# Kernel optimization log

Measured on AMD Instinct MI355X. Metric: run time of the kernel, lower is better.

Reference implementation:

```python
import jax, jax.numpy as jnp
import numpy as np


def fps(xyz, npoint):
    # farthest point sampling, starts at index 0 (matches pointnet2 CUDA kernel)
    B, N, _ = xyz.shape
    def step(carry, _):
        min_d, last = carry
        last_xyz = jnp.take_along_axis(xyz, last[:, None, None], axis=1)  # [B,1,3]
        d = jnp.sum((xyz - last_xyz) ** 2, axis=-1)                        # [B,N]
        min_d = jnp.minimum(min_d, d)
        nxt = jnp.argmax(min_d, axis=1).astype(jnp.int32)
        return (min_d, nxt), last
    init = (jnp.full((B, N), 1e10, xyz.dtype), jnp.zeros((B,), jnp.int32))
    _, idx = jax.lax.scan(step, init, None, length=npoint)
    return jnp.transpose(idx)  # [B, npoint]


def ball_query(xyz, new_xyz, radius, nsample):
    # first nsample points within radius; pad with first hit (0 if none) -- CUDA semantics
    N = xyz.shape[1]
    d2 = jnp.sum((new_xyz[:, :, None, :] - xyz[:, None, :, :]) ** 2, axis=-1)  # [B,S,N]
    cand = jnp.where(d2 < radius * radius, jnp.arange(N, dtype=jnp.int32)[None, None, :], N)
    srt = jnp.sort(cand, axis=-1)[..., :nsample]
    first = srt[..., :1]
    first = jnp.where(first == N, 0, first)
    return jnp.where(srt == N, first, srt)  # [B,S,K]


def gather_nbrs(x, idx):
    # x [B,N,C], idx [B,S,K] -> [B,S,K,C]
    B, S, K = idx.shape
    flat = jnp.take_along_axis(x, idx.reshape(B, S * K, 1), axis=1)
    return flat.reshape(B, S, K, x.shape[-1])


def shared_mlp(x, layers):
    # 1x1 conv (+ folded eval-mode BN) + ReLU per layer
    for w, b in layers:
        x = jax.nn.relu(jnp.einsum('bskc,oc->bsko', x, w) + b)
    return x


def sa_module(xyz, feat, npoint, radius, nsample, layers):
    idx = fps(xyz, npoint)
    new_xyz = jnp.take_along_axis(xyz, idx[:, :, None], axis=1)  # [B,S,3]
    gidx = ball_query(xyz, new_xyz, radius, nsample)
    grouped = gather_nbrs(xyz, gidx) - new_xyz[:, :, None, :]    # centered local xyz
    if feat is not None:
        grouped = jnp.concatenate([grouped, gather_nbrs(feat, gidx)], axis=-1)
    x = shared_mlp(grouped, layers)
    return new_xyz, jnp.max(x, axis=2)  # max-pool over neighbors -> [B,S,Cout]


def sa_module_all(xyz, feat, layers):
    # GroupAll: concat raw (uncentered) xyz with features, one group of all points
    x = jnp.concatenate([xyz, feat], axis=-1)[:, None]  # [B,1,N,3+C]
    x = shared_mlp(x, layers)
    return jnp.max(x, axis=2)[:, 0]  # [B,Cout]


def _forward(data, ws):
    B, T, N, _ = data.shape
    xyz = data.reshape(B * T, N, 3)
    xyz, feat = sa_module(xyz, None, 256, 0.2, 32, ws[0])
    xyz, feat = sa_module(xyz, feat, 128, 0.4, 32, ws[1])
    out = sa_module_all(xyz, feat, ws[2])
    return out.reshape(B, T, -1)


DIMS = [(3, 64), (64, 64), (64, 128), (131, 128), (128, 128), (128, 256), (259, 256), (256, 512), (512, 1024)]
NAMES = ['1_0', '1_1', '1_2', '2_0', '2_1', '2_2', '3_0', '3_1', '3_2']


def setup_inputs() -> dict:
    key = jax.random.key(0)
    keys = jax.random.split(key, 1 + 2 * len(DIMS))
    inp = {'data': jax.random.normal(keys[0], (4, 8, 4096, 3), jnp.float32)}
    for i, ((cin, cout), nm) in enumerate(zip(DIMS, NAMES)):
        inp['w' + nm] = jax.random.normal(keys[1 + 2 * i], (cout, cin), jnp.float32) / np.sqrt(cin).astype(np.float32)
        inp['b' + nm] = jax.random.normal(keys[2 + 2 * i], (cout,), jnp.float32) * 0.02
    return inp


def reference(data, w1_0, b1_0, w1_1, b1_1, w1_2, b1_2,
              w2_0, b2_0, w2_1, b2_1, w2_2, b2_2,
              w3_0, b3_0, w3_1, b3_1, w3_2, b3_2):
    ws = [[(w1_0, b1_0), (w1_1, b1_1), (w1_2, b1_2)],
          [(w2_0, b2_0), (w2_1, b2_1), (w2_2, b2_2)],
          [(w3_0, b3_0), (w3_1, b3_1), (w3_2, b3_2)]]
    return _forward(data, ws)
```

## Files before the change

kernel.cpp:

```cpp
#include <hip/hip_runtime.h>
#include <hip/hip_bf16.h>
#include <cstdint>
#include <cstddef>

#define BT 32
#define N1 4096
#define S1 256
#define S2 128
#define KNB 32

typedef __attribute__((ext_vector_type(8))) short short8;
typedef __attribute__((ext_vector_type(4))) float f32x4;

__device__ __forceinline__ float sqdist(float ax, float ay, float az,
                                        float bx, float by, float bz) {
    float dx = __fsub_rn(ax, bx), dy = __fsub_rn(ay, by), dz = __fsub_rn(az, bz);
    return __fadd_rn(__fadd_rn(__fmul_rn(dx, dx), __fmul_rn(dy, dy)), __fmul_rn(dz, dz));
}

__device__ __forceinline__ unsigned short f2bf(float f) {
    unsigned u = __float_as_uint(f);
    return (unsigned short)((u + 0x7FFFu + ((u >> 16) & 1u)) >> 16);
}
__device__ __forceinline__ float bf2f(unsigned short h) {
    return __uint_as_float(((unsigned)h) << 16);
}

__device__ __forceinline__ unsigned long long packvi(float v, int idx) {
    return ((unsigned long long)__float_as_uint(v) << 32) | (unsigned)(~idx);
}

template <int CTRL>
__device__ __forceinline__ unsigned long long dppmax(unsigned long long v) {
    int lo = (int)(unsigned)(v & 0xFFFFFFFFull);
    int hi = (int)(unsigned)(v >> 32);
    int lo2 = __builtin_amdgcn_update_dpp(0, lo, CTRL, 0xF, 0xF, false);
    int hi2 = __builtin_amdgcn_update_dpp(0, hi, CTRL, 0xF, 0xF, false);
    unsigned long long o = ((unsigned long long)(unsigned)hi2 << 32) | (unsigned)lo2;
    return o > v ? o : v;
}
template <int CTRL>
__device__ __forceinline__ void redstep(unsigned long long& v, float& x, float& y, float& z) {
    int lo2 = __builtin_amdgcn_update_dpp(0, (int)(unsigned)(v & 0xFFFFFFFFull), CTRL, 0xF, 0xF, false);
    int hi2 = __builtin_amdgcn_update_dpp(0, (int)(unsigned)(v >> 32), CTRL, 0xF, 0xF, false);
    int x2 = __builtin_amdgcn_update_dpp(0, __float_as_int(x), CTRL, 0xF, 0xF, false);
    int y2 = __builtin_amdgcn_update_dpp(0, __float_as_int(y), CTRL, 0xF, 0xF, false);
    int z2 = __builtin_amdgcn_update_dpp(0, __float_as_int(z), CTRL, 0xF, 0xF, false);
    unsigned long long o = ((unsigned long long)(unsigned)hi2 << 32) | (unsigned)(unsigned)lo2;
    if (o > v) { v = o; x = __int_as_float(x2); y = __int_as_float(y2); z = __int_as_float(z2); }
}
#define ROR1 0x121
#define ROR2 0x122
#define ROR4 0x124
#define ROR8 0x128

__global__ __launch_bounds__(256) void fps1_kernel(const float* __restrict__ xyz,
                                                   float* __restrict__ nxz,
                                                   float* __restrict__ nxz2) {
    const int b = blockIdx.x, tid = threadIdx.x;
    const int lane = tid & 63, wv = tid >> 6;
    const float* X = xyz + (size_t)b * (N1 * 3);
    __shared__ float4 s4[N1];
    __shared__ unsigned long long slots_v[2][16];
    __shared__ float4 slots_c[2][16];
    __shared__ float hist[S1 * 3];
    __shared__ float4 shist[S1];
    float px[16], py[16], pz[16], md[16];
    int bidx[16];
#pragma unroll
    for (int j = 0; j < 16; ++j) {
        int i = tid + 256 * j;
        float x = X[i * 3 + 0], y = X[i * 3 + 1], z = X[i * 3 + 2];
        s4[i] = make_float4(x, y, z, 0.f);
        px[j] = x; py[j] = y; pz[j] = z;
        md[j] = 1e10f;
        bidx[j] = i;
    }
    if (tid == 0) { hist[0] = X[0]; hist[1] = X[1]; hist[2] = X[2]; }
    __syncthreads();
    float lx = X[0], ly = X[1], lz = X[2];
    for (int t = 1; t < S1; ++t) {
        float bv = -1.0f; int bi = 0;
#pragma unroll
        for (int j = 0; j < 16; ++j) {
            float d = sqdist(px[j], py[j], pz[j], lx, ly, lz);
            float m = fminf(md[j], d);
            md[j] = m;
            if (m > bv) { bv = m; bi = bidx[j]; }
        }
        unsigned long long best = packvi(bv, bi);
        best = dppmax<ROR1>(best);
        best = dppmax<ROR2>(best);
        best = dppmax<ROR4>(best);
        best = dppmax<ROR8>(best);
        if ((lane & 15) == 0) {
            int vi = (int)(~(unsigned)best);
            slots_v[t & 1][wv * 4 + (lane >> 4)] = best;
            slots_c[t & 1][wv * 4 + (lane >> 4)] = s4[vi];
        }
        __syncthreads();
        unsigned long long v = slots_v[t & 1][lane & 15];
        float4 c = slots_c[t & 1][lane & 15];
        float x = c.x, y = c.y, z = c.z;
        redstep<ROR1>(v, x, y, z);
        redstep<ROR2>(v, x, y, z);
        redstep<ROR4>(v, x, y, z);
        redstep<ROR8>(v, x, y, z);
        lx = x; ly = y; lz = z;
        if (tid == 0) { hist[t * 3 + 0] = lx; hist[t * 3 + 1] = ly; hist[t * 3 + 2] = lz; }
    }
    __syncthreads();
    for (int u = tid; u < S1 * 3; u += 256) nxz[(size_t)b * S1 * 3 + u] = hist[u];
    if (wv == 0) {
        float p2x[4], p2y[4], p2z[4], m2[4];
        int b2i[4];
#pragma unroll
        for (int j = 0; j < 4; ++j) {
            int i = lane + 64 * j;
            float x = hist[i * 3 + 0], y = hist[i * 3 + 1], z = hist[i * 3 + 2];
            shist[i] = make_float4(x, y, z, 0.f);
            p2x[j] = x; p2y[j] = y; p2z[j] = z;
            m2[j] = 1e10f;
            b2i[j] = i;
        }
        if (lane == 0) {
            nxz2[(size_t)b * S2 * 3 + 0] = hist[0];
            nxz2[(size_t)b * S2 * 3 + 1] = hist[1];
            nxz2[(size_t)b * S2 * 3 + 2] = hist[2];
        }
        float cx = hist[0], cy = hist[1], cz = hist[2];
        for (int t = 1; t < S2; ++t) {
            float bv = -1.0f; int bi = 0;
#pragma unroll
            for (int j = 0; j < 4; ++j) {
                float d = sqdist(p2x[j], p2y[j], p2z[j], cx, cy, cz);
                float m = fminf(m2[j], d);
                m2[j] = m;
                if (m > bv) { bv = m; bi = b2i[j]; }
            }
            unsigned long long best = packvi(bv, bi);
            best = dppmax<ROR1>(best);
            best = dppmax<ROR2>(best);
            best = dppmax<ROR4>(best);
            best = dppmax<ROR8>(best);
            { unsigned long long o = __shfl_xor(best, 16); best = o > best ? o : best; }
            { unsigned long long o = __shfl_xor(best, 32); best = o > best ? o : best; }
            int vi = (int)(~(unsigned)best);
            float4 c = shist[vi];
            cx = c.x; cy = c.y; cz = c.z;
            if (lane == 0) {
                float* dst = nxz2 + ((size_t)b * S2 + t) * 3;
                dst[0] = cx; dst[1] = cy; dst[2] = cz;
            }
        }
    }
}

__global__ __launch_bounds__(256) void ballq1_kernel(const float* __restrict__ xyz,
                                                     const float* __restrict__ nxz,
                                                     int* __restrict__ gidx) {
    const int wid = (blockIdx.x * 256 + threadIdx.x) >> 6;
    const int lane = threadIdx.x & 63;
    const int b = wid >> 8;
    const float* X = xyz + (size_t)b * (N1 * 3);
    const float* C = nxz + (size_t)wid * 3;
    const float cx = C[0], cy = C[1], cz = C[2];
    const float r2 = (float)(0.2 * 0.2);
    int* G = gidx + (size_t)wid * KNB;
    int cnt = 0, first = 0;
    bool found = false;
    for (int j0 = 0; j0 < N1 && cnt < KNB; j0 += 64) {
        int j = j0 + lane;
        float d2 = sqdist(cx, cy, cz, X[j * 3 + 0], X[j * 3 + 1], X[j * 3 + 2]);
        bool hit = d2 < r2;
        unsigned long long mask = __ballot(hit);
        if (!found && mask) { first = j0 + __builtin_ctzll(mask); found = true; }
        if (hit) {
            int pos = cnt + __popcll(mask & ((1ull << lane) - 1ull));
            if (pos < KNB) G[pos] = j;
        }
        cnt += __popcll(mask);
    }
    if (cnt < KNB) {
        int pad = found ? first : 0;
        if (lane >= cnt && lane < KNB) G[lane] = pad;
    }
}

__global__ __launch_bounds__(256) void ballq2_kernel(const float* __restrict__ xyz1,
                                                     const float* __restrict__ nxz2,
                                                     int* __restrict__ gidx) {
    const int wid = (blockIdx.x * 256 + threadIdx.x) >> 6;
    const int lane = threadIdx.x & 63;
    const int b = wid >> 7;
    const float* X = xyz1 + (size_t)b * (S1 * 3);
    const float* C = nxz2 + (size_t)wid * 3;
    const float cx = C[0], cy = C[1], cz = C[2];
    const float r2 = (float)(0.4 * 0.4);
    int* G = gidx + (size_t)wid * KNB;
    int cnt = 0, first = 0;
    bool found = false;
    for (int j0 = 0; j0 < S1 && cnt < KNB; j0 += 64) {
        int j = j0 + lane;
        float d2 = sqdist(cx, cy, cz, X[j * 3 + 0], X[j * 3 + 1], X[j * 3 + 2]);
        bool hit = d2 < r2;
        unsigned long long mask = __ballot(hit);
        if (!found && mask) { first = j0 + __builtin_ctzll(mask); found = true; }
        if (hit) {
            int pos = cnt + __popcll(mask & ((1ull << lane) - 1ull));
            if (pos < KNB) G[pos] = j;
        }
        cnt += __popcll(mask);
    }
    if (cnt < KNB) {
        int pad = found ? first : 0;
        if (lane >= cnt && lane < KNB) G[lane] = pad;
    }
}

__global__ __launch_bounds__(256) void wconv_kernel(
    const float* __restrict__ w11, const float* __restrict__ w12,
    const float* __restrict__ w20, const float* __restrict__ w21,
    const float* __restrict__ w22, const float* __restrict__ w30,
    const float* __restrict__ w31, const float* __restrict__ w32,
    unsigned short* __restrict__ wb) {
    int u = blockIdx.x * 256 + threadIdx.x;
    if (u >= 823296) return;
    const float* src; int base, Kp, Ko; int perm = 0;
    if      (u < 4096)   { src = w11; base = 0;      Kp = 64;  Ko = 64;  }
    else if (u < 12288)  { src = w12; base = 4096;   Kp = 64;  Ko = 64;  }
    else if (u < 36864)  { src = w20; base = 12288;  Kp = 192; Ko = 131; perm = 128; }
    else if (u < 53248)  { src = w21; base = 36864;  Kp = 128; Ko = 128; }
    else if (u < 86016)  { src = w22; base = 53248;  Kp = 128; Ko = 128; }
    else if (u < 167936) { src = w30; base = 86016;  Kp = 320; Ko = 259; perm = 256; }
    else if (u < 299008) { src = w31; base = 167936; Kp = 256; Ko = 256; }
    else                 { src = w32; base = 299008; Kp = 512; Ko = 512; }
    int local = u - base;
    int n = local / Kp, k = local - n * Kp;
    float v;
    if (perm) {
        int ksrc = (k < perm) ? (k + 3) : ((k < perm + 3) ? (k - perm) : -1);
        v = (ksrc >= 0) ? src[(size_t)n * Ko + ksrc] : 0.f;
    } else {
        v = (k < Ko) ? src[(size_t)n * Ko + k] : 0.f;
    }
    wb[u] = f2bf(v);
}

__global__ __launch_bounds__(256) void m1_kernel(
    const float* __restrict__ xyz, const float* __restrict__ nxz,
    const int* __restrict__ g1,
    const float* __restrict__ w10, const float* __restrict__ b10,
    const unsigned short* __restrict__ w11b, const float* __restrict__ b11,
    const unsigned short* __restrict__ w12b, const float* __restrict__ b12,
    unsigned short* __restrict__ f1) {
    constexpr int AP = 72;
    __shared__ __align__(16) unsigned short As[128 * AP];
    __shared__ __align__(16) unsigned short Hs[128 * AP];
    __shared__ __align__(16) unsigned short Bs[128 * AP];
    __shared__ float sxyz[128 * 3];
    const int t = threadIdx.x;
    const int lane = t & 63, w = t >> 6;
    const int r16 = lane & 15, q = lane >> 4;
    const int m0 = blockIdx.x * 128;

    if (t < 128) {
        int row = m0 + t, bs = row >> 5, b = bs >> 8, j = g1[row];
        const float* P = xyz + ((size_t)b * N1 + j) * 3;
        const float* Cc = nxz + (size_t)bs * 3;
        sxyz[t * 3 + 0] = P[0] - Cc[0];
        sxyz[t * 3 + 1] = P[1] - Cc[1];
        sxyz[t * 3 + 2] = P[2] - Cc[2];
    }
    for (int c = t; c < 64 * 8; c += 256) {
        int row = c >> 3, ch = c & 7;
        *(short8*)&Bs[row * AP + ch * 8] = *(const short8*)&w11b[row * 64 + ch * 8];
    }
    __syncthreads();
    {
        const int r = t >> 1, half = (t & 1) * 32;
        const float x = sxyz[r * 3 + 0], y = sxyz[r * 3 + 1], z = sxyz[r * 3 + 2];
        unsigned short tmp[32];
#pragma unroll
        for (int o = 0; o < 32; ++o) {
            int oo = half + o;
            float acc = b10[oo];
            acc = fmaf(x, w10[oo * 3 + 0], acc);
            acc = fmaf(y, w10[oo * 3 + 1], acc);
            acc = fmaf(z, w10[oo * 3 + 2], acc);
            tmp[o] = f2bf(fmaxf(acc, 0.f));
        }
#pragma unroll
        for (int c2 = 0; c2 < 4; ++c2)
            *(short8*)&As[r * AP + half + c2 * 8] = *(short8*)&tmp[c2 * 8];
    }
    __syncthreads();
    {
        f32x4 acc[2][4];
#pragma unroll
        for (int i = 0; i < 2; ++i)
#pragma unroll
            for (int j = 0; j < 4; ++j) acc[i][j] = (f32x4){0.f, 0.f, 0.f, 0.f};
#pragma unroll
        for (int kk = 0; kk < 64; kk += 32) {
            short8 a0 = *(const short8*)&As[(w * 32 + r16) * AP + kk + q * 8];
            short8 a1 = *(const short8*)&As[(w * 32 + 16 + r16) * AP + kk + q * 8];
#pragma unroll
            for (int j = 0; j < 4; ++j) {
                short8 bf = *(const short8*)&Bs[(j * 16 + r16) * AP + kk + q * 8];
                acc[0][j] = __builtin_amdgcn_mfma_f32_16x16x32_bf16(a0, bf, acc[0][j], 0, 0, 0);
                acc[1][j] = __builtin_amdgcn_mfma_f32_16x16x32_bf16(a1, bf, acc[1][j], 0, 0, 0);
            }
        }
#pragma unroll
        for (int i = 0; i < 2; ++i)
#pragma unroll
            for (int j = 0; j < 4; ++j) {
                int col = j * 16 + r16;
                float bv = b11[col];
#pragma unroll
                for (int r = 0; r < 4; ++r) {
                    int row = w * 32 + i * 16 + q * 4 + r;
                    Hs[row * AP + col] = f2bf(fmaxf(acc[i][j][r] + bv, 0.f));
                }
            }
    }
    __syncthreads();
    for (int c = t; c < 128 * 8; c += 256) {
        int row = c >> 3, ch = c & 7;
        *(short8*)&Bs[row * AP + ch * 8] = *(const short8*)&w12b[row * 64 + ch * 8];
    }
    __syncthreads();
    {
        f32x4 acc[2][8];
#pragma unroll
        for (int i = 0; i < 2; ++i)
#pragma unroll
            for (int j = 0; j < 8; ++j) acc[i][j] = (f32x4){0.f, 0.f, 0.f, 0.f};
#pragma unroll
        for (int kk = 0; kk < 64; kk += 32) {
            short8 a0 = *(const short8*)&Hs[(w * 32 + r16) * AP + kk + q * 8];
            short8 a1 = *(const short8*)&Hs[(w * 32 + 16 + r16) * AP + kk + q * 8];
#pragma unroll
            for (int j = 0; j < 8; ++j) {
                short8 bf = *(const short8*)&Bs[(j * 16 + r16) * AP + kk + q * 8];
                acc[0][j] = __builtin_amdgcn_mfma_f32_16x16x32_bf16(a0, bf, acc[0][j], 0, 0, 0);
                acc[1][j] = __builtin_amdgcn_mfma_f32_16x16x32_bf16(a1, bf, acc[1][j], 0, 0, 0);
            }
        }
#pragma unroll
        for (int j = 0; j < 8; ++j) {
            int col = j * 16 + r16;
            float bv = b12[col];
            float mv = 0.f;
#pragma unroll
            for (int i = 0; i < 2; ++i)
#pragma unroll
                for (int r = 0; r < 4; ++r)
                    mv = fmaxf(mv, acc[i][j][r] + bv);
            mv = fmaxf(mv, __shfl_xor(mv, 16));
            mv = fmaxf(mv, __shfl_xor(mv, 32));
            if (q == 0)
                f1[(size_t)((m0 >> 5) + w) * 128 + col] = f2bf(mv);
        }
    }
}

__global__ __launch_bounds__(256) void m2_kernel(
    const float* __restrict__ xyz1, const float* __restrict__ nxz2,
    const int* __restrict__ g2, const unsigned short* __restrict__ f1,
    const unsigned short* __restrict__ w20p, const float* __restrict__ b20,
    const unsigned short* __restrict__ w21b, const float* __restrict__ b21,
    const unsigned short* __restrict__ w22b, const float* __restrict__ b22,
    unsigned short* __restrict__ f2) {
    constexpr int AP = 72, HP = 136;
    __shared__ __align__(16) unsigned short smem[36864];
    unsigned short* R1 = smem;
    unsigned short* R2 = smem + 18432;
    unsigned short* As = R1;
    unsigned short* Bs = R1 + 9216;
    unsigned short* H1 = R2;
    unsigned short* H2 = R1;
    unsigned short* Bs2 = R2;
    __shared__ int ribase[128];
    __shared__ unsigned short sxb[128 * 3];
    const int t = threadIdx.x;
    const int lane = t & 63, w = t >> 6;
    const int r16 = lane & 15, q = lane >> 4;
    const int m0 = blockIdx.x * 128;

    if (t < 128) {
        int row = m0 + t, bs = row >> 5, b = bs >> 7, j = g2[row];
        ribase[t] = (b * 256 + j) * 128;
        const float* P = xyz1 + ((size_t)b * S1 + j) * 3;
        const float* Cc = nxz2 + (size_t)bs * 3;
        sxb[t * 3 + 0] = f2bf(P[0] - Cc[0]);
        sxb[t * 3 + 1] = f2bf(P[1] - Cc[1]);
        sxb[t * 3 + 2] = f2bf(P[2] - Cc[2]);
    }
    __syncthreads();

    f32x4 acc[2][8];
#pragma unroll
    for (int i = 0; i < 2; ++i)
#pragma unroll
        for (int j = 0; j < 8; ++j) acc[i][j] = (f32x4){0.f, 0.f, 0.f, 0.f};
    for (int kt = 0; kt < 3; ++kt) {
        const int k0 = kt * 64;
        if (kt < 2) {
            for (int c = t; c < 128 * 8; c += 256) {
                int row = c >> 3, ch = c & 7;
                *(short8*)&As[row * AP + ch * 8] =
                    *(const short8*)&f1[(size_t)ribase[row] + k0 + ch * 8];
            }
        } else {
            for (int c = t; c < 128 * 8; c += 256) {
                int row = c >> 3, ch = c & 7;
                short8 v = (short8){0, 0, 0, 0, 0, 0, 0, 0};
                if (ch == 0) {
                    v[0] = (short)sxb[row * 3 + 0];
                    v[1] = (short)sxb[row * 3 + 1];
                    v[2] = (short)sxb[row * 3 + 2];
                }
                *(short8*)&As[row * AP + ch * 8] = v;
            }
        }
        for (int c = t; c < 128 * 8; c += 256) {
            int row = c >> 3, ch = c & 7;
            *(short8*)&Bs[row * AP + ch * 8] =
                *(const short8*)&w20p[(size_t)row * 192 + k0 + ch * 8];
        }
        __syncthreads();
#pragma unroll
        for (int kk = 0; kk < 64; kk += 32) {
            short8 a0 = *(const short8*)&As[(w * 32 + r16) * AP + kk + q * 8];
            short8 a1 = *(const short8*)&As[(w * 32 + 16 + r16) * AP + kk + q * 8];
#pragma unroll
            for (int j = 0; j < 8; ++j) {
                short8 bf = *(const short8*)&Bs[(j * 16 + r16) * AP + kk + q * 8];
                acc[0][j] = __builtin_amdgcn_mfma_f32_16x16x32_bf16(a0, bf, acc[0][j], 0, 0, 0);
                acc[1][j] = __builtin_amdgcn_mfma_f32_16x16x32_bf16(a1, bf, acc[1][j], 0, 0, 0);
            }
        }
        __syncthreads();
    }
#pragma unroll
    for (int i = 0; i < 2; ++i)
#pragma unroll
        for (int j = 0; j < 8; ++j) {
            int col = j * 16 + r16;
            float bv = b20[col];
#pragma unroll
            for (int r = 0; r < 4; ++r) {
                int row = w * 32 + i * 16 + q * 4 + r;
                H1[row * HP + col] = f2bf(fmaxf(acc[i][j][r] + bv, 0.f));
            }
        }
    __syncthreads();

#pragma unroll
    for (int i = 0; i < 2; ++i)
#pragma unroll
        for (int j = 0; j < 8; ++j) acc[i][j] = (f32x4){0.f, 0.f, 0.f, 0.f};
    for (int kt = 0; kt < 2; ++kt) {
        const int k0 = kt * 64;
        for (int c = t; c < 128 * 8; c += 256) {
            int row = c >> 3, ch = c & 7;
            *(short8*)&As[row * AP + ch * 8] =
                *(const short8*)&w21b[(size_t)row * 128 + k0 + ch * 8];
        }
        __syncthreads();
#pragma unroll
        for (int kk = 0; kk < 64; kk += 32) {
            short8 a0 = *(const short8*)&H1[(w * 32 + r16) * HP + k0 + kk + q * 8];
            short8 a1 = *(const short8*)&H1[(w * 32 + 16 + r16) * HP + k0 + kk + q * 8];
#pragma unroll
            for (int j = 0; j < 8; ++j) {
                short8 bf = *(const short8*)&As[(j * 16 + r16) * AP + kk + q * 8];
                acc[0][j] = __builtin_amdgcn_mfma_f32_16x16x32_bf16(a0, bf, acc[0][j], 0, 0, 0);
                acc[1][j] = __builtin_amdgcn_mfma_f32_16x16x32_bf16(a1, bf, acc[1][j], 0, 0, 0);
            }
        }
        __syncthreads();
    }
#pragma unroll
    for (int i = 0; i < 2; ++i)
#pragma unroll
        for (int j = 0; j < 8; ++j) {
            int col = j * 16 + r16;
            float bv = b21[col];
#pragma unroll
            for (int r = 0; r < 4; ++r) {
                int row = w * 32 + i * 16 + q * 4 + r;
                H2[row * HP + col] = f2bf(fmaxf(acc[i][j][r] + bv, 0.f));
            }
        }
    __syncthreads();

    f32x4 acc2[2][16];
#pragma unroll
    for (int i = 0; i < 2; ++i)
#pragma unroll
        for (int j = 0; j < 16; ++j) acc2[i][j] = (f32x4){0.f, 0.f, 0.f, 0.f};
    for (int kt = 0; kt < 2; ++kt) {
        const int k0 = kt * 64;
        for (int c = t; c < 256 * 8; c += 256) {
            int row = c >> 3, ch = c & 7;
            *(short8*)&Bs2[row * AP + ch * 8] =
                *(const short8*)&w22b[(size_t)row * 128 + k0 + ch * 8];
        }
        __syncthreads();
#pragma unroll
        for (int kk = 0; kk < 64; kk += 32) {
            short8 a0 = *(const short8*)&H2[(w * 32 + r16) * HP + k0 + kk + q * 8];
            short8 a1 = *(const short8*)&H2[(w * 32 + 16 + r16) * HP + k0 + kk + q * 8];
#pragma unroll
            for (int j = 0; j < 16; ++j) {
                short8 bf = *(const short8*)&Bs2[(j * 16 + r16) * AP + kk + q * 8];
                acc2[0][j] = __builtin_amdgcn_mfma_f32_16x16x32_bf16(a0, bf, acc2[0][j], 0, 0, 0);
                acc2[1][j] = __builtin_amdgcn_mfma_f32_16x16x32_bf16(a1, bf, acc2[1][j], 0, 0, 0);
            }
        }
        __syncthreads();
    }
#pragma unroll
    for (int j = 0; j < 16; ++j) {
        int col = j * 16 + r16;
        float bv = b22[col];
        float mv = 0.f;
#pragma unroll
        for (int i = 0; i < 2; ++i)
#pragma unroll
            for (int r = 0; r < 4; ++r)
                mv = fmaxf(mv, acc2[i][j][r] + bv);
        mv = fmaxf(mv, __shfl_xor(mv, 16));
        mv = fmaxf(mv, __shfl_xor(mv, 32));
        if (q == 0)
            f2[(size_t)((m0 >> 5) + w) * 256 + col] = f2bf(mv);
    }
}

__global__ __launch_bounds__(256) void l30_kernel(
    const float* __restrict__ nxz2, const unsigned short* __restrict__ f2,
    const unsigned short* __restrict__ w30p, const float* __restrict__ bias,
    unsigned short* __restrict__ C) {
    constexpr int AP = 72;
    __shared__ __align__(16) unsigned short As[128 * AP];
    __shared__ __align__(16) unsigned short Bs[128 * AP];
    const int t = threadIdx.x;
    const int lane = t & 63, w = t >> 6;
    const int r16 = lane & 15, q = lane >> 4;
    const int m0 = blockIdx.x * 128;
    const int n0 = blockIdx.y * 128;

    f32x4 acc[2][8];
#pragma unroll
    for (int i = 0; i < 2; ++i)
#pragma unroll
        for (int j = 0; j < 8; ++j) acc[i][j] = (f32x4){0.f, 0.f, 0.f, 0.f};

    for (int kt = 0; kt < 5; ++kt) {
        const int k0 = kt * 64;
        if (kt < 4) {
            for (int c = t; c < 128 * 8; c += 256) {
                int row = c >> 3, ch = c & 7;
                *(short8*)&As[row * AP + ch * 8] =
                    *(const short8*)&f2[(size_t)(m0 + row) * 256 + k0 + ch * 8];
            }
        } else {
            for (int c = t; c < 128 * 8; c += 256) {
                int row = c >> 3, ch = c & 7;
                short8 v = (short8){0, 0, 0, 0, 0, 0, 0, 0};
                if (ch == 0) {
                    const float* P = nxz2 + (size_t)(m0 + row) * 3;
                    v[0] = (short)f2bf(P[0]);
                    v[1] = (short)f2bf(P[1]);
                    v[2] = (short)f2bf(P[2]);
                }
                *(short8*)&As[row * AP + ch * 8] = v;
            }
        }
        for (int c = t; c < 128 * 8; c += 256) {
            int row = c >> 3, ch = c & 7;
            *(short8*)&Bs[row * AP + ch * 8] =
                *(const short8*)&w30p[(size_t)(n0 + row) * 320 + k0 + ch * 8];
        }
        __syncthreads();
#pragma unroll
        for (int kk = 0; kk < 64; kk += 32) {
            short8 a0 = *(const short8*)&As[(w * 32 + r16) * AP + kk + q * 8];
            short8 a1 = *(const short8*)&As[(w * 32 + 16 + r16) * AP + kk + q * 8];
#pragma unroll
            for (int j = 0; j < 8; ++j) {
                short8 bf = *(const short8*)&Bs[(j * 16 + r16) * AP + kk + q * 8];
                acc[0][j] = __builtin_amdgcn_mfma_f32_16x16x32_bf16(a0, bf, acc[0][j], 0, 0, 0);
                acc[1][j] = __builtin_amdgcn_mfma_f32_16x16x32_bf16(a1, bf, acc[1][j], 0, 0, 0);
            }
        }
        __syncthreads();
    }
#pragma unroll
    for (int i = 0; i < 2; ++i)
#pragma unroll
        for (int j = 0; j < 8; ++j) {
            int col = n0 + j * 16 + r16;
            float bv = bias[col];
#pragma unroll
            for (int r = 0; r < 4; ++r) {
                int row = m0 + w * 32 + i * 16 + q * 4 + r;
                C[(size_t)row * 256 + col] = f2bf(fmaxf(acc[i][j][r] + bv, 0.f));
            }
        }
}

template <int BM_>
__global__ __launch_bounds__(256) void mfma_gemm(const unsigned short* __restrict__ X,
                                                 const unsigned short* __restrict__ W,
                                                 const float* __restrict__ bias,
                                                 unsigned short* __restrict__ C,
                                                 int M, int N, int K) {
    constexpr int BK = 64, AP = BK + 8;
    constexpr int RW = BM_ / 64;
    constexpr int WR = BM_ / 4;
    __shared__ __align__(16) unsigned short As[BM_ * AP];
    __shared__ __align__(16) unsigned short Bs[128 * AP];
    const int t = threadIdx.x;
    const int lane = t & 63, w = t >> 6;
    const int m0 = blockIdx.x * BM_;
    const int n0 = blockIdx.y * 128;
    const int r16 = lane & 15, q = lane >> 4;

    f32x4 acc[RW][8];
#pragma unroll
    for (int i = 0; i < RW; ++i)
#pragma unroll
        for (int j = 0; j < 8; ++j) acc[i][j] = (f32x4){0.f, 0.f, 0.f, 0.f};

    for (int k0 = 0; k0 < K; k0 += BK) {
        for (int c = t; c < BM_ * 8; c += 256) {
            int row = c >> 3, ch = c & 7;
            *(short8*)&As[row * AP + ch * 8] =
                *(const short8*)&X[(size_t)(m0 + row) * K + k0 + ch * 8];
        }
        for (int c = t; c < 128 * 8; c += 256) {
            int row = c >> 3, ch = c & 7;
            *(short8*)&Bs[row * AP + ch * 8] =
                *(const short8*)&W[(size_t)(n0 + row) * K + k0 + ch * 8];
        }
        __syncthreads();
#pragma unroll
        for (int kk = 0; kk < BK; kk += 32) {
            short8 a[RW];
#pragma unroll
            for (int i = 0; i < RW; ++i)
                a[i] = *(const short8*)&As[(w * WR + i * 16 + r16) * AP + kk + q * 8];
#pragma unroll
            for (int j = 0; j < 8; ++j) {
                short8 bf = *(const short8*)&Bs[(j * 16 + r16) * AP + kk + q * 8];
#pragma unroll
                for (int i = 0; i < RW; ++i)
                    acc[i][j] = __builtin_amdgcn_mfma_f32_16x16x32_bf16(a[i], bf, acc[i][j], 0, 0, 0);
            }
        }
        __syncthreads();
    }
#pragma unroll
    for (int i = 0; i < RW; ++i)
#pragma unroll
        for (int j = 0; j < 8; ++j) {
            int col = n0 + j * 16 + r16;
            float bv = bias[col];
#pragma unroll
            for (int r = 0; r < 4; ++r) {
                int row = m0 + w * WR + i * 16 + q * 4 + r;
                C[(size_t)row * N + col] = f2bf(fmaxf(acc[i][j][r] + bv, 0.f));
            }
        }
}

__global__ __launch_bounds__(256) void gemm_pool128(const unsigned short* __restrict__ X,
                                                    const unsigned short* __restrict__ W,
                                                    const float* __restrict__ bias,
                                                    float* __restrict__ out) {
    constexpr int BK = 64, AP = BK + 8, K = 512;
    __shared__ __align__(16) unsigned short As[128 * AP];
    __shared__ __align__(16) unsigned short Bs[128 * AP];
    __shared__ float pool[4][128];
    const int t = threadIdx.x;
    const int lane = t & 63, w = t >> 6;
    const int m0 = blockIdx.x * 128;
    const int n0 = blockIdx.y * 128;
    const int r16 = lane & 15, q = lane >> 4;

    f32x4 acc[2][8];
#pragma unroll
    for (int i = 0; i < 2; ++i)
#pragma unroll
        for (int j = 0; j < 8; ++j) acc[i][j] = (f32x4){0.f, 0.f, 0.f, 0.f};

    for (int k0 = 0; k0 < K; k0 += BK) {
        for (int c = t; c < 128 * 8; c += 256) {
            int row = c >> 3, ch = c & 7;
            *(short8*)&As[row * AP + ch * 8] =
                *(const short8*)&X[(size_t)(m0 + row) * K + k0 + ch * 8];
        }
        for (int c = t; c < 128 * 8; c += 256) {
            int row = c >> 3, ch = c & 7;
            *(short8*)&Bs[row * AP + ch * 8] =
                *(const short8*)&W[(size_t)(n0 + row) * K + k0 + ch * 8];
        }
        __syncthreads();
#pragma unroll
        for (int kk = 0; kk < BK; kk += 32) {
            short8 a0 = *(const short8*)&As[(w * 32 + r16) * AP + kk + q * 8];
            short8 a1 = *(const short8*)&As[(w * 32 + 16 + r16) * AP + kk + q * 8];
#pragma unroll
            for (int j = 0; j < 8; ++j) {
                short8 bf = *(const short8*)&Bs[(j * 16 + r16) * AP + kk + q * 8];
                acc[0][j] = __builtin_amdgcn_mfma_f32_16x16x32_bf16(a0, bf, acc[0][j], 0, 0, 0);
                acc[1][j] = __builtin_amdgcn_mfma_f32_16x16x32_bf16(a1, bf, acc[1][j], 0, 0, 0);
            }
        }
        __syncthreads();
    }
#pragma unroll
    for (int j = 0; j < 8; ++j) {
        float bv = bias[n0 + j * 16 + r16];
        float mv = 0.f;
#pragma unroll
        for (int i = 0; i < 2; ++i)
#pragma unroll
            for (int r = 0; r < 4; ++r)
                mv = fmaxf(mv, acc[i][j][r] + bv);
        mv = fmaxf(mv, __shfl_xor(mv, 16));
        mv = fmaxf(mv, __shfl_xor(mv, 32));
        if (q == 0) pool[w][j * 16 + r16] = mv;
    }
    __syncthreads();
    if (t < 128) {
        float m = fmaxf(fmaxf(pool[0][t], pool[1][t]), fmaxf(pool[2][t], pool[3][t]));
        out[(size_t)blockIdx.x * 1024 + n0 + t] = m;
    }
}

extern "C" void kernel_launch(void* const* d_in, const int* in_sizes, int n_in,
                              void* d_out, int out_size, void* d_ws, size_t ws_size,
                              hipStream_t stream) {
    const float* data = (const float*)d_in[0];
    const float* w10 = (const float*)d_in[1];  const float* b10 = (const float*)d_in[2];
    const float* w11 = (const float*)d_in[3];  const float* b11 = (const float*)d_in[4];
    const float* w12 = (const float*)d_in[5];  const float* b12 = (const float*)d_in[6];
    const float* w20 = (const float*)d_in[7];  const float* b20 = (const float*)d_in[8];
    const float* w21 = (const float*)d_in[9];  const float* b21 = (const float*)d_in[10];
    const float* w22 = (const float*)d_in[11]; const float* b22 = (const float*)d_in[12];
    const float* w30 = (const float*)d_in[13]; const float* b30 = (const float*)d_in[14];
    const float* w31 = (const float*)d_in[15]; const float* b31 = (const float*)d_in[16];
    const float* w32 = (const float*)d_in[17]; const float* b32 = (const float*)d_in[18];
    float* out = (float*)d_out;

    char* ws = (char*)d_ws;
    size_t off = 0;
    auto alloc = [&](size_t bytes) -> void* {
        void* p = ws + off;
        off += (bytes + 255) & ~(size_t)255;
        return p;
    };
    float* nxz1 = (float*)alloc((size_t)BT * S1 * 3 * 4);
    int*   g1   = (int*)  alloc((size_t)BT * S1 * KNB * 4);
    float* nxz2 = (float*)alloc((size_t)BT * S2 * 3 * 4);
    int*   g2   = (int*)  alloc((size_t)BT * S2 * KNB * 4);
    unsigned short* wb  = (unsigned short*)alloc((size_t)823296 * 2);
    unsigned short* f1  = (unsigned short*)alloc((size_t)8192 * 128 * 2);
    unsigned short* f2  = (unsigned short*)alloc((size_t)4096 * 256 * 2);
    unsigned short* C1  = (unsigned short*)alloc((size_t)4096 * 256 * 2);
    unsigned short* C2  = (unsigned short*)alloc((size_t)4096 * 512 * 2);

    const unsigned short* w11b = wb + 0;
    const unsigned short* w12b = wb + 4096;
    const unsigned short* w20p = wb + 12288;
    const unsigned short* w21b = wb + 36864;
    const unsigned short* w22b = wb + 53248;
    const unsigned short* w30p = wb + 86016;
    const unsigned short* w31b = wb + 167936;
    const unsigned short* w32b = wb + 299008;

    wconv_kernel<<<(823296 + 255) / 256, 256, 0, stream>>>(w11, w12, w20, w21, w22, w30, w31, w32, wb);

    fps1_kernel<<<BT, 256, 0, stream>>>(data, nxz1, nxz2);
    ballq1_kernel<<<(BT * S1) / 4, 256, 0, stream>>>(data, nxz1, g1);
    m1_kernel<<<262144 / 128, 256, 0, stream>>>(data, nxz1, g1, w10, b10, w11b, b11, w12b, b12, f1);
    ballq2_kernel<<<(BT * S2) / 4, 256, 0, stream>>>(nxz1, nxz2, g2);
    m2_kernel<<<131072 / 128, 256, 0, stream>>>(nxz1, nxz2, g2, f1, w20p, b20, w21b, b21, w22b, b22, f2);
    l30_kernel<<<dim3(4096 / 128, 2), 256, 0, stream>>>(nxz2, f2, w30p, b30, C1);
    mfma_gemm<64><<<dim3(4096 / 64, 4), 256, 0, stream>>>(C1, w31b, b31, C2, 4096, 512, 256);
    gemm_pool128<<<dim3(4096 / 128, 8), 256, 0, stream>>>(C2, w32b, b32, out);
}
```

Before: 512.9 us.

## Split second-stage FPS into its own kernel and simplify cross-wave argmax

```diff
diff --git a/kernel.cpp b/kernel.cpp
--- a/kernel.cpp
+++ b/kernel.cpp
@@ -39,32 +39,19 @@
     unsigned long long o = ((unsigned long long)(unsigned)hi2 << 32) | (unsigned)lo2;
     return o > v ? o : v;
 }
-template <int CTRL>
-__device__ __forceinline__ void redstep(unsigned long long& v, float& x, float& y, float& z) {
-    int lo2 = __builtin_amdgcn_update_dpp(0, (int)(unsigned)(v & 0xFFFFFFFFull), CTRL, 0xF, 0xF, false);
-    int hi2 = __builtin_amdgcn_update_dpp(0, (int)(unsigned)(v >> 32), CTRL, 0xF, 0xF, false);
-    int x2 = __builtin_amdgcn_update_dpp(0, __float_as_int(x), CTRL, 0xF, 0xF, false);
-    int y2 = __builtin_amdgcn_update_dpp(0, __float_as_int(y), CTRL, 0xF, 0xF, false);
-    int z2 = __builtin_amdgcn_update_dpp(0, __float_as_int(z), CTRL, 0xF, 0xF, false);
-    unsigned long long o = ((unsigned long long)(unsigned)hi2 << 32) | (unsigned)(unsigned)lo2;
-    if (o > v) { v = o; x = __int_as_float(x2); y = __int_as_float(y2); z = __int_as_float(z2); }
-}
 #define ROR1 0x121
 #define ROR2 0x122
 #define ROR4 0x124
 #define ROR8 0x128
 
 __global__ __launch_bounds__(256) void fps1_kernel(const float* __restrict__ xyz,
-                                                   float* __restrict__ nxz,
-                                                   float* __restrict__ nxz2) {
+                                                   float* __restrict__ nxz) {
     const int b = blockIdx.x, tid = threadIdx.x;
     const int lane = tid & 63, wv = tid >> 6;
     const float* X = xyz + (size_t)b * (N1 * 3);
     __shared__ float4 s4[N1];
-    __shared__ unsigned long long slots_v[2][16];
-    __shared__ float4 slots_c[2][16];
+    __shared__ unsigned long long slots[2][16];
     __shared__ float hist[S1 * 3];
-    __shared__ float4 shist[S1];
     float px[16], py[16], pz[16], md[16];
     int bidx[16];
 #pragma unroll
@@ -78,7 +65,8 @@
     }
     if (tid == 0) { hist[0] = X[0]; hist[1] = X[1]; hist[2] = X[2]; }
     __syncthreads();
-    float lx = X[0], ly = X[1], lz = X[2];
+    float4 c0 = s4[0];
+    float lx = c0.x, ly = c0.y, lz = c0.z;
     for (int t = 1; t < S1; ++t) {
         float bv = -1.0f; int bi = 0;
 #pragma unroll
@@ -93,65 +81,67 @@
         best = dppmax<ROR2>(best);
         best = dppmax<ROR4>(best);
         best = dppmax<ROR8>(best);
-        if ((lane & 15) == 0) {
-            int vi = (int)(~(unsigned)best);
-            slots_v[t & 1][wv * 4 + (lane >> 4)] = best;
-            slots_c[t & 1][wv * 4 + (lane >> 4)] = s4[vi];
-        }
-        __syncthreads();
-        unsigned long long v = slots_v[t & 1][lane & 15];
-        float4 c = slots_c[t & 1][lane & 15];
-        float x = c.x, y = c.y, z = c.z;
-        redstep<ROR1>(v, x, y, z);
-        redstep<ROR2>(v, x, y, z);
-        redstep<ROR4>(v, x, y, z);
-        redstep<ROR8>(v, x, y, z);
-        lx = x; ly = y; lz = z;
+        if ((lane & 15) == 0) slots[t & 1][wv * 4 + (lane >> 4)] = best;
+        __syncthreads();
+        unsigned long long w = slots[t & 1][lane & 15];
+        w = dppmax<ROR1>(w);
+        w = dppmax<ROR2>(w);
+        w = dppmax<ROR4>(w);
+        w = dppmax<ROR8>(w);
+        int vi = (int)(~(unsigned)w);
+        float4 c = s4[vi];
+        lx = c.x; ly = c.y; lz = c.z;
         if (tid == 0) { hist[t * 3 + 0] = lx; hist[t * 3 + 1] = ly; hist[t * 3 + 2] = lz; }
     }
     __syncthreads();
     for (int u = tid; u < S1 * 3; u += 256) nxz[(size_t)b * S1 * 3 + u] = hist[u];
-    if (wv == 0) {
-        float p2x[4], p2y[4], p2z[4], m2[4];
-        int b2i[4];
+}
+
+__global__ __launch_bounds__(64) void fps2_kernel(const float* __restrict__ xyz1,
+                                                  float* __restrict__ nxz2) {
+    const int b = blockIdx.x, lane = threadIdx.x;
+    const float* X = xyz1 + (size_t)b * (S1 * 3);
+    __shared__ float4 s4[S1];
+    float px[4], py[4], pz[4], md[4];
+    int bidx[4];
+#pragma unroll
+    for (int j = 0; j < 4; ++j) {
+        int i = lane + 64 * j;
+        float x = X[i * 3 + 0], y = X[i * 3 + 1], z = X[i * 3 + 2];
+        s4[i] = make_float4(x, y, z, 0.f);
+        px[j] = x; py[j] = y; pz[j] = z;
+        md[j] = 1e10f;
+        bidx[j] = i;
+    }
+    if (lane == 0) {
+        nxz2[(size_t)b * S2 * 3 + 0] = X[0];
+        nxz2[(size_t)b * S2 * 3 + 1] = X[1];
+        nxz2[(size_t)b * S2 * 3 + 2] = X[2];
+    }
+    float4 cc = s4[0];
+    float lx = cc.x, ly = cc.y, lz = cc.z;
+    for (int t = 1; t < S2; ++t) {
+        float bv = -1.0f; int bi = 0;
 #pragma unroll
         for (int j = 0; j < 4; ++j) {
-            int i = lane + 64 * j;
-            float x = hist[i * 3 + 0], y = hist[i * 3 + 1], z = hist[i * 3 + 2];
-            shist[i] = make_float4(x, y, z, 0.f);
-            p2x[j] = x; p2y[j] = y; p2z[j] = z;
-            m2[j] = 1e10f;
-            b2i[j] = i;
-        }
+            float d = sqdist(px[j], py[j], pz[j], lx, ly, lz);
+            float m = fminf(md[j], d);
+            md[j] = m;
+            if (m > bv) { bv = m; bi = bidx[j]; }
+        }
+        unsigned long long best = packvi(bv, bi);
+        best = dppmax<ROR1>(best);
+        best = dppmax<ROR2>(best);
+        best = dppmax<ROR4>(best);
+        best = dppmax<ROR8>(best);
+        { unsigned long long o = __shfl_xor(best, 16); best = o > best ? o : best; }
+        { unsigned long long o = __shfl_xor(best, 32); best = o > best ? o : best; }
+        int vi = (int)(~(unsigned)best);
+        float4 c = s4[vi];
+        lx = c.x; ly = c.y; lz = c.z;
         if (lane == 0) {
-            nxz2[(size_t)b * S2 * 3 + 0] = hist[0];
-            nxz2[(size_t)b * S2 * 3 + 1] = hist[1];
-            nxz2[(size_t)b * S2 * 3 + 2] = hist[2];
-        }
-        float cx = hist[0], cy = hist[1], cz = hist[2];
-        for (int t = 1; t < S2; ++t) {
-            float bv = -1.0f; int bi = 0;
-#pragma unroll
-            for (int j = 0; j < 4; ++j) {
-                float d = sqdist(p2x[j], p2y[j], p2z[j], cx, cy, cz);
-                float m = fminf(m2[j], d);
-                m2[j] = m;
-                if (m > bv) { bv = m; bi = b2i[j]; }
-            }
-            unsigned long long best = packvi(bv, bi);
-            best = dppmax<ROR1>(best);
-            best = dppmax<ROR2>(best);
-            best = dppmax<ROR4>(best);
-            best = dppmax<ROR8>(best);
-            { unsigned long long o = __shfl_xor(best, 16); best = o > best ? o : best; }
-            { unsigned long long o = __shfl_xor(best, 32); best = o > best ? o : best; }
-            int vi = (int)(~(unsigned)best);
-            float4 c = shist[vi];
-            cx = c.x; cy = c.y; cz = c.z;
-            if (lane == 0) {
-                float* dst = nxz2 + ((size_t)b * S2 + t) * 3;
-                dst[0] = cx; dst[1] = cy; dst[2] = cz;
-            }
+            float* dst = nxz2 + ((size_t)b * S2 + t) * 3;
+            dst[0] = lx; dst[1] = ly; dst[2] = lz;
         }
     }
 }
@@ -786,9 +776,10 @@
 
     wconv_kernel<<<(823296 + 255) / 256, 256, 0, stream>>>(w11, w12, w20, w21, w22, w30, w31, w32, wb);
 
-    fps1_kernel<<<BT, 256, 0, stream>>>(data, nxz1, nxz2);
+    fps1_kernel<<<BT, 256, 0, stream>>>(data, nxz1);
     ballq1_kernel<<<(BT * S1) / 4, 256, 0, stream>>>(data, nxz1, g1);
     m1_kernel<<<262144 / 128, 256, 0, stream>>>(data, nxz1, g1, w10, b10, w11b, b11, w12b, b12, f1);
+    fps2_kernel<<<BT, 64, 0, stream>>>(nxz1, nxz2);
     ballq2_kernel<<<(BT * S2) / 4, 256, 0, stream>>>(nxz1, nxz2, g2);
     m2_kernel<<<131072 / 128, 256, 0, stream>>>(nxz1, nxz2, g2, f1, w20p, b20, w21b, b21, w22b, b22, f2);
     l30_kernel<<<dim3(4096 / 128, 2), 256, 0, stream>>>(nxz2, f2, w30p, b30, C1);
```

Result: faster. 486.1 us (-5.2%).
